# Optimization experiments

Measured on AMD Instinct MI355X. Metric: run time of the kernel, lower is better.

## Reference

```python
import jax, jax.numpy as jnp
import numpy as np

N = 50000      # nodes
E = 800000     # edges (avg degree 16)
DIN = 500      # input_dim
HID = 100      # hid_dim (fixed in module)
DOUT = 64      # output_dim
EPS = 1e-5     # LayerNorm eps (torch default)


def _layer_norm(x, g, b):
    mu = jnp.mean(x, axis=-1, keepdims=True)
    var = jnp.var(x, axis=-1, keepdims=True)
    return (x - mu) / jnp.sqrt(var + EPS) * g + b


def _gcn_conv(x, src, tgt, W, b):
    # PyG GCNConv: self-loops + symmetric normalization + linear + scatter-add
    h = x @ W  # [N, out]
    idx = jnp.arange(N)
    src_sl = jnp.concatenate([src, idx])
    tgt_sl = jnp.concatenate([tgt, idx])
    deg = jax.ops.segment_sum(jnp.ones(src_sl.shape, h.dtype), tgt_sl, num_segments=N)
    dinv = jnp.where(deg > 0, deg ** -0.5, 0.0)
    norm = dinv[src_sl] * dinv[tgt_sl]  # [E+N]
    out = jax.ops.segment_sum(h[src_sl] * norm[:, None], tgt_sl, num_segments=N)
    return out + b


def setup_inputs() -> dict:
    key = jax.random.key(0)
    ks = jax.random.split(key, 10)
    glorot = lambda k, fi, fo: jax.random.normal(k, (fi, fo), jnp.float32) * np.float32(1.0 / np.sqrt(fi))
    z = lambda d: jnp.zeros((d,), jnp.float32)
    return dict(
        data_x=jax.random.normal(ks[0], (N, DIN), jnp.float32),
        data_edge_index=jax.random.randint(ks[1], (2, E), 0, N),
        data_edge_attr=jnp.zeros((E,), jnp.int32),  # single relation type
        t_W1=glorot(ks[2], DIN, HID), t_b1=z(HID), t_g1=jnp.ones((HID,), jnp.float32), t_be1=z(HID),
        t_W2=glorot(ks[3], HID, HID), t_b2=z(HID), t_g2=jnp.ones((HID,), jnp.float32), t_be2=z(HID),
        r_Wrel=glorot(ks[4], HID, HID)[None],  # [n_relations=1, H, H]
        r_Wself=glorot(ks[5], HID, HID), r_b=z(HID),
        c1_W=glorot(ks[6], HID, HID), c1_b=z(HID),
        c2_W=glorot(ks[7], HID, DOUT), c2_b=z(DOUT),
    )


def reference(data_x, data_edge_index, data_edge_attr,
              t_W1, t_b1, t_g1, t_be1, t_W2, t_b2, t_g2, t_be2,
              r_Wrel, r_Wself, r_b, c1_W, c1_b, c2_W, c2_b):
    src, tgt = data_edge_index[0], data_edge_index[1]
    # transform: Linear -> LN -> ReLU -> Linear -> LN -> ReLU
    x = jax.nn.relu(_layer_norm(data_x @ t_W1 + t_b1, t_g1, t_be1))
    x = jax.nn.relu(_layer_norm(x @ t_W2 + t_b2, t_g2, t_be2))
    # RGCN, n_relations=1, n_layers=1: per-relation message + self transform
    msgs = x[src] @ r_Wrel[0]  # edge_attr is all relation 0
    x = x @ r_Wself + jax.ops.segment_sum(msgs, tgt, num_segments=N) + r_b
    x = jax.nn.relu(x)  # dropout = identity (eval)
    x = jax.nn.relu(_gcn_conv(x, src, tgt, c1_W, c1_b))
    x = _gcn_conv(x, src, tgt, c2_W, c2_b)
    return jax.nn.log_softmax(x, axis=1)
```

## Files before the change

### kernel.cpp

```cpp
#include <hip/hip_runtime.h>
#include <hip/hip_bf16.h>

typedef __attribute__((ext_vector_type(8))) short short8;
typedef __attribute__((ext_vector_type(8))) unsigned short ushort8;
typedef __attribute__((ext_vector_type(4))) float f32x4;

static constexpr int NN = 50000;
static constexpr int NE = 800000;
static constexpr int SCAN_B = 196;
static constexpr int NBLK = (NN + 63) / 64;

#define MFMA16x16x32 __builtin_amdgcn_mfma_f32_16x16x32_bf16

__device__ __forceinline__ float b2f(unsigned short u){
  unsigned v = ((unsigned)u) << 16;
  return __builtin_bit_cast(float, v);
}
__device__ __forceinline__ unsigned short f2b(float f){
  unsigned x = __builtin_bit_cast(unsigned, f);
  unsigned r = (x + 0x7fffu + ((x >> 16) & 1u)) >> 16;
  return (unsigned short)r;
}
__device__ __forceinline__ short8 u2s(ushort8 v){
  return __builtin_bit_cast(short8, v);
}

__device__ __align__(256) int   g_isf32;
__device__ __align__(256) unsigned short g_W1t  [112 * 512];
__device__ __align__(256) unsigned short g_W2t  [112 * 128];
__device__ __align__(256) unsigned short g_WselfT[112 * 128];
__device__ __align__(256) unsigned short g_WrelT [112 * 128];
__device__ __align__(256) unsigned short g_c1Wt [112 * 128];
__device__ __align__(256) unsigned short g_c2Wt [64 * 128];
__device__ __align__(256) unsigned short g_bufA[(size_t)NN * 128];
__device__ __align__(256) unsigned short g_bufB[(size_t)NN * 128];
__device__ __align__(256) unsigned short g_bufC[(size_t)NN * 128];
__device__ __align__(256) int   g_deg[NN];
__device__ __align__(256) int   g_rowptr[NN + 1];
__device__ __align__(256) int   g_cursor[NN];
__device__ __align__(256) int   g_colidx[NE];
__device__ __align__(256) float g_dinv[NN];
__device__ __align__(256) int   g_partial[256];

__device__ __forceinline__ float ld_in(const void* p, int idx, int isf32){
  if (isf32) return ((const float*)p)[idx];
  return b2f(((const unsigned short*)p)[idx]);
}

__global__ void k_detect_zero(const unsigned short* __restrict__ x){
  if (blockIdx.x == 0){
    __shared__ int sh[256];
    int tid = threadIdx.x;
    int cnt = 0;
    for (int j = 0; j < 16; j++){
      unsigned short h = x[(size_t)(tid * 16 + j) * 2];
      int e = (h >> 7) & 0xFF;
      if (e >= 90 && e <= 160) cnt++;
    }
    sh[tid] = cnt;
    __syncthreads();
    for (int off = 128; off > 0; off >>= 1){
      if (tid < off) sh[tid] += sh[tid + off];
      __syncthreads();
    }
    if (tid == 0) g_isf32 = (sh[0] < 2458) ? 1 : 0;
  } else {
    int i = (blockIdx.x - 1) * 256 + threadIdx.x;
    if (i < NN){ g_deg[i] = 0; g_cursor[i] = 0; }
  }
}

__device__ __forceinline__ void xp_one(const void* W, unsigned short* Wt, int idx,
                                       int K, int Nc, int Kpad, int isf32){
  int n = idx / Kpad;
  int k = idx - n * Kpad;
  float v = 0.f;
  if (n < Nc && k < K) v = ld_in(W, k * Nc + n, isf32);
  Wt[idx] = f2b(v);
}
__global__ void k_transpose_all(const void* W1, const void* W2, const void* Wself,
                                const void* Wrel, const void* c1W, const void* c2W){
  int idx = blockIdx.x * 256 + threadIdx.x;
  const int isf32 = g_isf32;
  if (idx < 57344){ xp_one(W1, g_W1t, idx, 500, 100, 512, isf32); return; }
  idx -= 57344;
  if (idx < 14336){ xp_one(W2,    g_W2t,    idx, 100, 100, 128, isf32); return; }
  idx -= 14336;
  if (idx < 14336){ xp_one(Wself, g_WselfT, idx, 100, 100, 128, isf32); return; }
  idx -= 14336;
  if (idx < 14336){ xp_one(Wrel,  g_WrelT,  idx, 100, 100, 128, isf32); return; }
  idx -= 14336;
  if (idx < 14336){ xp_one(c1W,   g_c1Wt,   idx, 100, 100, 128, isf32); return; }
  idx -= 14336;
  if (idx < 8192){  xp_one(c2W,   g_c2Wt,   idx, 100, 64,  128, isf32); }
}

__global__ void k_deg(const int* __restrict__ tgt){
  int e = blockIdx.x * 256 + threadIdx.x;
  if (e < NE) atomicAdd(&g_deg[tgt[e]], 1);
}
__global__ __launch_bounds__(256) void k_scan1(){
  __shared__ int sh[256];
  int t = threadIdx.x;
  int i = blockIdx.x * 256 + t;
  int val = (i < NN) ? g_deg[i] : 0;
  sh[t] = val; __syncthreads();
#pragma unroll
  for (int off = 1; off < 256; off <<= 1){
    int v = (t >= off) ? sh[t - off] : 0;
    __syncthreads(); sh[t] += v; __syncthreads();
  }
  if (i < NN){ g_rowptr[i] = sh[t] - val; g_dinv[i] = rsqrtf((float)(val + 1)); }
  if (t == 255) g_partial[blockIdx.x] = sh[255];
}
__global__ __launch_bounds__(256) void k_scan2(){
  __shared__ int sh[256];
  int t = threadIdx.x;
  int val = (t < SCAN_B) ? g_partial[t] : 0;
  sh[t] = val; __syncthreads();
#pragma unroll
  for (int off = 1; off < 256; off <<= 1){
    int v = (t >= off) ? sh[t - off] : 0;
    __syncthreads(); sh[t] += v; __syncthreads();
  }
  if (t < SCAN_B) g_partial[t] = sh[t] - val;
  if (t == 255) g_rowptr[NN] = sh[255];
}
__global__ __launch_bounds__(256) void k_scan3(){
  int i = blockIdx.x * 256 + threadIdx.x;
  if (i < NN) g_rowptr[i] += g_partial[blockIdx.x];
}
__global__ void k_fill(const int* __restrict__ src, const int* __restrict__ tgt){
  int e = blockIdx.x * 256 + threadIdx.x;
  if (e >= NE) return;
  int t = tgt[e];
  int pos = g_rowptr[t] + atomicAdd(&g_cursor[t], 1);
  g_colidx[pos] = src[e];
}


template<int DO_LN>
__device__ __forceinline__ void wave_epi(const f32x4* acc, unsigned short* dst,
    int rstride, int grow0, int lane, int isf32,
    const void* bias, const void* gm, const void* be){
  const int m = lane & 15;
  const int q = lane >> 4;
  float bf_[7], gf_[7], ef_[7];
#pragma unroll
  for (int t = 0; t < 7; t++){
    int col = t * 16 + m;
    bool ok = col < 100;
    bf_[t] = ok ? ld_in(bias, col, isf32) : 0.f;
    if (DO_LN){
      gf_[t] = ok ? ld_in(gm, col, isf32) : 0.f;
      ef_[t] = ok ? ld_in(be, col, isf32) : 0.f;
    }
  }
#pragma unroll
  for (int r = 0; r < 4; r++){
    int rl = q * 4 + r;
    float vals[7], s1 = 0.f, s2 = 0.f;
#pragma unroll
    for (int t = 0; t < 7; t++){
      int col = t * 16 + m;
      float v = (col < 100) ? (acc[t][r] + bf_[t]) : 0.f;
      vals[t] = v; s1 += v; s2 += v * v;
    }
    if (DO_LN){
#pragma unroll
      for (int msk = 1; msk < 16; msk <<= 1){
        s1 += __shfl_xor(s1, msk, 64);
        s2 += __shfl_xor(s2, msk, 64);
      }
      float mu = s1 * 0.01f;
      float var = fmaxf(s2 * 0.01f - mu * mu, 0.f);
      float rstd = rsqrtf(var + 1e-5f);
#pragma unroll
      for (int t = 0; t < 7; t++)
        vals[t] = (vals[t] - mu) * rstd * gf_[t] + ef_[t];
    }
    if (grow0 + rl < NN){
      unsigned short* orow = dst + (size_t)rl * rstride;
#pragma unroll
      for (int t = 0; t < 7; t++){
        int col = t * 16 + m;
        float y = fmaxf(vals[t], 0.f);
        orow[col] = f2b((col < 100) ? y : 0.f);
      }
      orow[112 + m] = 0;
    }
  }
}

template<int MODE>
__device__ __forceinline__ void agg_tile(const unsigned short* __restrict__ x,
    unsigned short* aggT, int tid, int brow0){
  const int nl = tid >> 2;
  const int c0 = (tid & 3) * 32;
  const int node = min(brow0 + nl, NN - 1);
  const float wt = (MODE != 0) ? g_dinv[node] : 1.f;
  float a[32];
#pragma unroll
  for (int k = 0; k < 32; k++) a[k] = 0.f;
  const int p0 = g_rowptr[node], p1 = g_rowptr[node + 1];
  for (int p = p0; p < p1; p += 2){
    int s0 = g_colidx[p];
    bool ok1 = (p + 1) < p1;
    int s1 = ok1 ? g_colidx[p + 1] : node;
    float w0 = (MODE != 0) ? g_dinv[s0] * wt : 1.f;
    float w1 = ok1 ? ((MODE != 0) ? g_dinv[s1] * wt : 1.f) : 0.f;
    ushort8 r0[4], r1[4];
#pragma unroll
    for (int u = 0; u < 4; u++){
      r0[u] = *reinterpret_cast<const ushort8*>(&x[(size_t)s0 * 128 + c0 + u * 8]);
      r1[u] = *reinterpret_cast<const ushort8*>(&x[(size_t)s1 * 128 + c0 + u * 8]);
    }
#pragma unroll
    for (int u = 0; u < 4; u++)
#pragma unroll
      for (int k = 0; k < 8; k++){
        a[u * 8 + k] += w0 * b2f((unsigned short)r0[u][k]);
        a[u * 8 + k] += w1 * b2f((unsigned short)r1[u][k]);
      }
  }
  if (MODE != 0){
    float ws = wt * wt;
#pragma unroll
    for (int u = 0; u < 4; u++){
      ushort8 sv = *reinterpret_cast<const ushort8*>(&x[(size_t)node * 128 + c0 + u * 8]);
#pragma unroll
      for (int k = 0; k < 8; k++) a[u * 8 + k] += ws * b2f((unsigned short)sv[k]);
    }
  }
  unsigned short* arow = aggT + nl * 136 + c0;
#pragma unroll
  for (int u = 0; u < 4; u++){
    ushort8 o;
#pragma unroll
    for (int k = 0; k < 8; k++) o[k] = f2b(a[u * 8 + k]);
    *reinterpret_cast<ushort8*>(&arow[u * 8]) = o;
  }
}


__global__ __launch_bounds__(256, 4) void k_gemm12(const void* __restrict__ Aext,
    const void* b1, const void* gm1, const void* be1,
    const void* b2, const void* gm2, const void* be2){
  __shared__ unsigned short xT[4][16][136];
  const int tid = threadIdx.x;
  const int w = tid >> 6, lane = tid & 63;
  const int m = lane & 15, q = lane >> 4;
  const int row0 = blockIdx.x * 64 + w * 16;
  const int isf32 = g_isf32;
  const int arow = min(row0 + m, NN - 1);

  f32x4 acc[7] = {};
  if (isf32){
    const float* base = (const float*)Aext + (size_t)arow * 500;
#pragma unroll 4
    for (int kc = 0; kc < 16; kc++){
      int col = kc * 32 + q * 8;
      f32x4 lo = *reinterpret_cast<const f32x4*>(base + min(col, 496));
      f32x4 hi = *reinterpret_cast<const f32x4*>(base + min(col + 4, 496));
      short8 a = {(short)f2b(lo[0]), (short)f2b(lo[1]), (short)f2b(lo[2]), (short)f2b(lo[3]),
                  (short)f2b(hi[0]), (short)f2b(hi[1]), (short)f2b(hi[2]), (short)f2b(hi[3])};
#pragma unroll
      for (int t = 0; t < 7; t++){
        short8 b = *reinterpret_cast<const short8*>(g_W1t + (size_t)(t * 16 + m) * 512 + col);
        acc[t] = MFMA16x16x32(a, b, acc[t], 0, 0, 0);
      }
    }
  } else {
    const unsigned short* base = (const unsigned short*)Aext + (size_t)arow * 500;
#pragma unroll 4
    for (int kc = 0; kc < 16; kc++){
      int col = kc * 32 + q * 8;
      ushort4 lo = *reinterpret_cast<const ushort4*>(base + min(col, 496));
      ushort4 hi = *reinterpret_cast<const ushort4*>(base + min(col + 4, 496));
      short8 a = {(short)lo.x, (short)lo.y, (short)lo.z, (short)lo.w,
                  (short)hi.x, (short)hi.y, (short)hi.z, (short)hi.w};
#pragma unroll
      for (int t = 0; t < 7; t++){
        short8 b = *reinterpret_cast<const short8*>(g_W1t + (size_t)(t * 16 + m) * 512 + col);
        acc[t] = MFMA16x16x32(a, b, acc[t], 0, 0, 0);
      }
    }
  }
  wave_epi<1>(acc, &xT[w][0][0], 136, 0, lane, isf32, b1, gm1, be1);
  __syncthreads();

  f32x4 acc2[7] = {};
#pragma unroll
  for (int kc = 0; kc < 4; kc++){
    int k0 = kc * 32 + q * 8;
    short8 a = u2s(*reinterpret_cast<const ushort8*>(&xT[w][m][k0]));
#pragma unroll
    for (int t = 0; t < 7; t++){
      short8 b = *reinterpret_cast<const short8*>(g_W2t + (size_t)(t * 16 + m) * 128 + k0);
      acc2[t] = MFMA16x16x32(a, b, acc2[t], 0, 0, 0);
    }
  }
  wave_epi<1>(acc2, g_bufB + (size_t)row0 * 128, 128, row0, lane, isf32, b2, gm2, be2);
}

__global__ __launch_bounds__(256, 4) void k_rgcn_f(const void* rb){
  __shared__ unsigned short aggT[64 * 136];
  const int tid = threadIdx.x;
  const int brow0 = blockIdx.x * 64;
  agg_tile<0>(g_bufB, aggT, tid, brow0);
  __syncthreads();

  const int w = tid >> 6, lane = tid & 63;
  const int m = lane & 15, q = lane >> 4;
  const int row0 = brow0 + w * 16;
  const int arow = min(row0 + m, NN - 1);
  const int isf32 = g_isf32;
  f32x4 acc[7] = {};
#pragma unroll
  for (int kc = 0; kc < 4; kc++){
    int k0 = kc * 32 + q * 8;
    short8 a1 = u2s(*reinterpret_cast<const ushort8*>(&g_bufB[(size_t)arow * 128 + k0]));
#pragma unroll
    for (int t = 0; t < 7; t++){
      short8 b = *reinterpret_cast<const short8*>(g_WselfT + (size_t)(t * 16 + m) * 128 + k0);
      acc[t] = MFMA16x16x32(a1, b, acc[t], 0, 0, 0);
    }
    short8 a2 = u2s(*reinterpret_cast<const ushort8*>(&aggT[(w * 16 + m) * 136 + k0]));
#pragma unroll
    for (int t = 0; t < 7; t++){
      short8 b = *reinterpret_cast<const short8*>(g_WrelT + (size_t)(t * 16 + m) * 128 + k0);
      acc[t] = MFMA16x16x32(a2, b, acc[t], 0, 0, 0);
    }
  }
  wave_epi<0>(acc, g_bufC + (size_t)row0 * 128, 128, row0, lane, isf32, rb, nullptr, nullptr);
}

__global__ __launch_bounds__(256, 4) void k_conv_f(const void* c1b){
  __shared__ unsigned short aggT[64 * 136];
  const int tid = threadIdx.x;
  const int brow0 = blockIdx.x * 64;
  agg_tile<1>(g_bufC, aggT, tid, brow0);
  __syncthreads();

  const int w = tid >> 6, lane = tid & 63;
  const int m = lane & 15, q = lane >> 4;
  const int row0 = brow0 + w * 16;
  const int isf32 = g_isf32;
  unsigned short* tile = aggT + w * 16 * 136;

  f32x4 acc[7] = {};
#pragma unroll
  for (int kc = 0; kc < 4; kc++){
    int k0 = kc * 32 + q * 8;
    short8 a = u2s(*reinterpret_cast<const ushort8*>(&tile[m * 136 + k0]));
#pragma unroll
    for (int t = 0; t < 7; t++){
      short8 b = *reinterpret_cast<const short8*>(g_c1Wt + (size_t)(t * 16 + m) * 128 + k0);
      acc[t] = MFMA16x16x32(a, b, acc[t], 0, 0, 0);
    }
  }
  __syncthreads();
  wave_epi<0>(acc, tile, 136, 0, lane, isf32, c1b, nullptr, nullptr);
  __syncthreads();

  f32x4 acc2[4] = {};
#pragma unroll
  for (int kc = 0; kc < 4; kc++){
    int k0 = kc * 32 + q * 8;
    short8 a = u2s(*reinterpret_cast<const ushort8*>(&tile[m * 136 + k0]));
#pragma unroll
    for (int t = 0; t < 4; t++){
      short8 b = *reinterpret_cast<const short8*>(g_c2Wt + (size_t)(t * 16 + m) * 128 + k0);
      acc2[t] = MFMA16x16x32(a, b, acc2[t], 0, 0, 0);
    }
  }
#pragma unroll
  for (int r = 0; r < 4; r++){
    int row = row0 + q * 4 + r;
    if (row < NN){
      unsigned short* orow = g_bufA + (size_t)row * 64;
#pragma unroll
      for (int t = 0; t < 4; t++) orow[t * 16 + m] = f2b(acc2[t][r]);
    }
  }
}

__global__ __launch_bounds__(256) void k_agg_lsm(const void* __restrict__ bias,
                                                 void* __restrict__ outv){
  const int isf32 = g_isf32;
  int node = blockIdx.x * 32 + (threadIdx.x >> 3);
  if (node >= NN) return;
  const int c8 = (threadIdx.x & 7) * 8;
  float wt = g_dinv[node];
  float a[4][8];
#pragma unroll
  for (int j = 0; j < 4; j++)
#pragma unroll
    for (int k = 0; k < 8; k++) a[j][k] = 0.f;
  int p0 = g_rowptr[node], p1 = g_rowptr[node + 1];
  for (int p = p0; p < p1; p += 4){
    int sj[4]; float wj[4];
#pragma unroll
    for (int j = 0; j < 4; j++){
      bool ok = (p + j) < p1;
      sj[j] = ok ? g_colidx[p + j] : node;
      wj[j] = ok ? g_dinv[sj[j]] * wt : 0.f;
    }
    ushort8 r[4];
#pragma unroll
    for (int j = 0; j < 4; j++)
      r[j] = *reinterpret_cast<const ushort8*>(&g_bufA[(size_t)sj[j] * 64 + c8]);
#pragma unroll
    for (int j = 0; j < 4; j++)
#pragma unroll
      for (int k = 0; k < 8; k++) a[j][k] += wj[j] * b2f((unsigned short)r[j][k]);
  }
  float ws = wt * wt;
  ushort8 sv = *reinterpret_cast<const ushort8*>(&g_bufA[(size_t)node * 64 + c8]);
#pragma unroll
  for (int k = 0; k < 8; k++) a[0][k] += ws * b2f((unsigned short)sv[k]);

  float v[8], mx = -1e30f;
#pragma unroll
  for (int k = 0; k < 8; k++){
    v[k] = a[0][k] + a[1][k] + a[2][k] + a[3][k] + ld_in(bias, c8 + k, isf32);
    mx = fmaxf(mx, v[k]);
  }
#pragma unroll
  for (int msk = 1; msk < 8; msk <<= 1) mx = fmaxf(mx, __shfl_xor(mx, msk, 64));
  float se = 0.f;
#pragma unroll
  for (int k = 0; k < 8; k++) se += expf(v[k] - mx);
#pragma unroll
  for (int msk = 1; msk < 8; msk <<= 1) se += __shfl_xor(se, msk, 64);
  float lse = logf(se);
  size_t ro = (size_t)node * 64 + c8;
  if (isf32){
    float* o = (float*)outv + ro;
#pragma unroll
    for (int k = 0; k < 8; k++) o[k] = v[k] - mx - lse;
  } else {
    unsigned short* o = (unsigned short*)outv + ro;
#pragma unroll
    for (int k = 0; k < 8; k++) o[k] = f2b(v[k] - mx - lse);
  }
}

extern "C" void kernel_launch(void* const* d_in, const int* in_sizes, int n_in,
                              void* d_out, int out_size, void* d_ws, size_t ws_size,
                              hipStream_t stream){
  (void)in_sizes; (void)n_in; (void)out_size; (void)d_ws; (void)ws_size;
  const void* data_x = d_in[0];
  const int* ei = (const int*)d_in[1];
  const int* src = ei;
  const int* tgt = ei + NE;
  const void *W1 = d_in[3], *b1 = d_in[4], *gm1 = d_in[5], *be1 = d_in[6];
  const void *W2 = d_in[7], *b2 = d_in[8], *gm2 = d_in[9], *be2 = d_in[10];
  const void *Wrel = d_in[11], *Wself = d_in[12], *rb = d_in[13];
  const void *c1W = d_in[14], *c1b = d_in[15];
  const void *c2W = d_in[16], *c2b = d_in[17];

  k_detect_zero<<<1 + (NN + 255) / 256, 256, 0, stream>>>((const unsigned short*)data_x);
  k_transpose_all<<<(122880 + 255) / 256, 256, 0, stream>>>(W1, W2, Wself, Wrel, c1W, c2W);

  k_deg<<<(NE + 255) / 256, 256, 0, stream>>>(tgt);
  k_scan1<<<SCAN_B, 256, 0, stream>>>();
  k_scan2<<<1, 256, 0, stream>>>();
  k_scan3<<<SCAN_B, 256, 0, stream>>>();
  k_fill<<<(NE + 255) / 256, 256, 0, stream>>>(src, tgt);

  k_gemm12<<<NBLK, 256, 0, stream>>>(data_x, b1, gm1, be1, b2, gm2, be2);
  k_rgcn_f<<<NBLK, 256, 0, stream>>>(rb);
  k_conv_f<<<NBLK, 256, 0, stream>>>(c1b);
  k_agg_lsm<<<(NN + 31) / 32, 256, 0, stream>>>(c2b, d_out);
}
```

Measured before the change: 480.9 us.

## Block weight layout by K, deepen gather unrolling, prefetch GEMM inputs, drop block barriers

The transposed weights are now stored in 32-wide K blocks, so each lane's B fragment loads come from a contiguous region. The edge-gather loops now issue four (fused GCN/RGCN tiles) or eight (final aggregation) neighbour rows per iteration, giving more loads in flight. The first GEMM preloads a whole chunk of A into registers behind a scheduling barrier. Block-wide __syncthreads are removed where each wave only touches its own LDS rows, and launch bounds drop from 4 to 3 blocks per CU to make room for the extra registers, which may reduce occupancy.

```diff
diff --git a/kernel.cpp b/kernel.cpp
--- a/kernel.cpp
+++ b/kernel.cpp
@@ -71,28 +71,28 @@
 }
 
 __device__ __forceinline__ void xp_one(const void* W, unsigned short* Wt, int idx,
-                                       int K, int Nc, int Kpad, int isf32){
+                                       int K, int Nc, int Kpad, int Npad, int isf32){
   int n = idx / Kpad;
   int k = idx - n * Kpad;
   float v = 0.f;
   if (n < Nc && k < K) v = ld_in(W, k * Nc + n, isf32);
-  Wt[idx] = f2b(v);
+  Wt[(k >> 5) * (Npad * 32) + n * 32 + (k & 31)] = f2b(v);
 }
 __global__ void k_transpose_all(const void* W1, const void* W2, const void* Wself,
                                 const void* Wrel, const void* c1W, const void* c2W){
   int idx = blockIdx.x * 256 + threadIdx.x;
   const int isf32 = g_isf32;
-  if (idx < 57344){ xp_one(W1, g_W1t, idx, 500, 100, 512, isf32); return; }
+  if (idx < 57344){ xp_one(W1, g_W1t, idx, 500, 100, 512, 112, isf32); return; }
   idx -= 57344;
-  if (idx < 14336){ xp_one(W2,    g_W2t,    idx, 100, 100, 128, isf32); return; }
+  if (idx < 14336){ xp_one(W2,    g_W2t,    idx, 100, 100, 128, 112, isf32); return; }
   idx -= 14336;
-  if (idx < 14336){ xp_one(Wself, g_WselfT, idx, 100, 100, 128, isf32); return; }
+  if (idx < 14336){ xp_one(Wself, g_WselfT, idx, 100, 100, 128, 112, isf32); return; }
   idx -= 14336;
-  if (idx < 14336){ xp_one(Wrel,  g_WrelT,  idx, 100, 100, 128, isf32); return; }
+  if (idx < 14336){ xp_one(Wrel,  g_WrelT,  idx, 100, 100, 128, 112, isf32); return; }
   idx -= 14336;
-  if (idx < 14336){ xp_one(c1W,   g_c1Wt,   idx, 100, 100, 128, isf32); return; }
+  if (idx < 14336){ xp_one(c1W,   g_c1Wt,   idx, 100, 100, 128, 112, isf32); return; }
   idx -= 14336;
-  if (idx < 8192){  xp_one(c2W,   g_c2Wt,   idx, 100, 64,  128, isf32); }
+  if (idx < 8192){  xp_one(c2W,   g_c2Wt,   idx, 100, 64,  128, 64, isf32); }
 }
 
 __global__ void k_deg(const int* __restrict__ tgt){
@@ -203,25 +203,27 @@
 #pragma unroll
   for (int k = 0; k < 32; k++) a[k] = 0.f;
   const int p0 = g_rowptr[node], p1 = g_rowptr[node + 1];
-  for (int p = p0; p < p1; p += 2){
-    int s0 = g_colidx[p];
-    bool ok1 = (p + 1) < p1;
-    int s1 = ok1 ? g_colidx[p + 1] : node;
-    float w0 = (MODE != 0) ? g_dinv[s0] * wt : 1.f;
-    float w1 = ok1 ? ((MODE != 0) ? g_dinv[s1] * wt : 1.f) : 0.f;
-    ushort8 r0[4], r1[4];
-#pragma unroll
-    for (int u = 0; u < 4; u++){
-      r0[u] = *reinterpret_cast<const ushort8*>(&x[(size_t)s0 * 128 + c0 + u * 8]);
-      r1[u] = *reinterpret_cast<const ushort8*>(&x[(size_t)s1 * 128 + c0 + u * 8]);
-    }
-#pragma unroll
-    for (int u = 0; u < 4; u++)
-#pragma unroll
-      for (int k = 0; k < 8; k++){
-        a[u * 8 + k] += w0 * b2f((unsigned short)r0[u][k]);
-        a[u * 8 + k] += w1 * b2f((unsigned short)r1[u][k]);
-      }
+  for (int p = p0; p < p1; p += 4){
+    int s[4]; float wj[4];
+#pragma unroll
+    for (int j = 0; j < 4; j++){
+      bool ok = (p + j) < p1;
+      s[j] = ok ? g_colidx[p + j] : node;
+      wj[j] = ok ? ((MODE != 0) ? g_dinv[s[j]] * wt : 1.f) : 0.f;
+    }
+    ushort8 r[4][4];
+#pragma unroll
+    for (int j = 0; j < 4; j++)
+#pragma unroll
+      for (int u = 0; u < 4; u++)
+        r[j][u] = *reinterpret_cast<const ushort8*>(&x[(size_t)s[j] * 128 + c0 + u * 8]);
+#pragma unroll
+    for (int j = 0; j < 4; j++)
+#pragma unroll
+      for (int u = 0; u < 4; u++)
+#pragma unroll
+        for (int k = 0; k < 8; k++)
+          a[u * 8 + k] += wj[j] * b2f((unsigned short)r[j][u][k]);
   }
   if (MODE != 0){
     float ws = wt * wt;
@@ -243,7 +245,7 @@
 }
 
 
-__global__ __launch_bounds__(256, 4) void k_gemm12(const void* __restrict__ Aext,
+__global__ __launch_bounds__(256, 3) void k_gemm12(const void* __restrict__ Aext,
     const void* b1, const void* gm1, const void* be1,
     const void* b2, const void* gm2, const void* be2){
   __shared__ unsigned short xT[4][16][136];
@@ -257,58 +259,74 @@
   f32x4 acc[7] = {};
   if (isf32){
     const float* base = (const float*)Aext + (size_t)arow * 500;
-#pragma unroll 4
+#pragma unroll
+    for (int h = 0; h < 2; h++){
+      f32x4 Ab[16];
+#pragma unroll
+      for (int kc = 0; kc < 8; kc++){
+        int col = (h * 8 + kc) * 32 + q * 8;
+        Ab[2 * kc]     = *reinterpret_cast<const f32x4*>(base + min(col, 496));
+        Ab[2 * kc + 1] = *reinterpret_cast<const f32x4*>(base + min(col + 4, 496));
+      }
+      __builtin_amdgcn_sched_barrier(0);
+#pragma unroll
+      for (int kc = 0; kc < 8; kc++){
+        f32x4 lo = Ab[2 * kc], hi = Ab[2 * kc + 1];
+        short8 a = {(short)f2b(lo[0]), (short)f2b(lo[1]), (short)f2b(lo[2]), (short)f2b(lo[3]),
+                    (short)f2b(hi[0]), (short)f2b(hi[1]), (short)f2b(hi[2]), (short)f2b(hi[3])};
+        const unsigned short* bp = g_W1t + (h * 8 + kc) * 3584 + m * 32 + q * 8;
+#pragma unroll
+        for (int t = 0; t < 7; t++){
+          short8 b = *reinterpret_cast<const short8*>(bp + t * 512);
+          acc[t] = MFMA16x16x32(a, b, acc[t], 0, 0, 0);
+        }
+      }
+    }
+  } else {
+    const unsigned short* base = (const unsigned short*)Aext + (size_t)arow * 500;
+    ushort4 Ab[32];
+#pragma unroll
     for (int kc = 0; kc < 16; kc++){
       int col = kc * 32 + q * 8;
-      f32x4 lo = *reinterpret_cast<const f32x4*>(base + min(col, 496));
-      f32x4 hi = *reinterpret_cast<const f32x4*>(base + min(col + 4, 496));
-      short8 a = {(short)f2b(lo[0]), (short)f2b(lo[1]), (short)f2b(lo[2]), (short)f2b(lo[3]),
-                  (short)f2b(hi[0]), (short)f2b(hi[1]), (short)f2b(hi[2]), (short)f2b(hi[3])};
+      Ab[2 * kc]     = *reinterpret_cast<const ushort4*>(base + min(col, 496));
+      Ab[2 * kc + 1] = *reinterpret_cast<const ushort4*>(base + min(col + 4, 496));
+    }
+    __builtin_amdgcn_sched_barrier(0);
+#pragma unroll
+    for (int kc = 0; kc < 16; kc++){
+      ushort4 lo = Ab[2 * kc], hi = Ab[2 * kc + 1];
+      short8 a = {(short)lo.x, (short)lo.y, (short)lo.z, (short)lo.w,
+                  (short)hi.x, (short)hi.y, (short)hi.z, (short)hi.w};
+      const unsigned short* bp = g_W1t + kc * 3584 + m * 32 + q * 8;
 #pragma unroll
       for (int t = 0; t < 7; t++){
-        short8 b = *reinterpret_cast<const short8*>(g_W1t + (size_t)(t * 16 + m) * 512 + col);
+        short8 b = *reinterpret_cast<const short8*>(bp + t * 512);
         acc[t] = MFMA16x16x32(a, b, acc[t], 0, 0, 0);
       }
     }
-  } else {
-    const unsigned short* base = (const unsigned short*)Aext + (size_t)arow * 500;
-#pragma unroll 4
-    for (int kc = 0; kc < 16; kc++){
-      int col = kc * 32 + q * 8;
-      ushort4 lo = *reinterpret_cast<const ushort4*>(base + min(col, 496));
-      ushort4 hi = *reinterpret_cast<const ushort4*>(base + min(col + 4, 496));
-      short8 a = {(short)lo.x, (short)lo.y, (short)lo.z, (short)lo.w,
-                  (short)hi.x, (short)hi.y, (short)hi.z, (short)hi.w};
-#pragma unroll
-      for (int t = 0; t < 7; t++){
-        short8 b = *reinterpret_cast<const short8*>(g_W1t + (size_t)(t * 16 + m) * 512 + col);
-        acc[t] = MFMA16x16x32(a, b, acc[t], 0, 0, 0);
-      }
-    }
   }
   wave_epi<1>(acc, &xT[w][0][0], 136, 0, lane, isf32, b1, gm1, be1);
-  __syncthreads();
 
   f32x4 acc2[7] = {};
 #pragma unroll
   for (int kc = 0; kc < 4; kc++){
     int k0 = kc * 32 + q * 8;
     short8 a = u2s(*reinterpret_cast<const ushort8*>(&xT[w][m][k0]));
+    const unsigned short* bp = g_W2t + kc * 3584 + m * 32 + q * 8;
 #pragma unroll
     for (int t = 0; t < 7; t++){
-      short8 b = *reinterpret_cast<const short8*>(g_W2t + (size_t)(t * 16 + m) * 128 + k0);
+      short8 b = *reinterpret_cast<const short8*>(bp + t * 512);
       acc2[t] = MFMA16x16x32(a, b, acc2[t], 0, 0, 0);
     }
   }
   wave_epi<1>(acc2, g_bufB + (size_t)row0 * 128, 128, row0, lane, isf32, b2, gm2, be2);
 }
 
-__global__ __launch_bounds__(256, 4) void k_rgcn_f(const void* rb){
+__global__ __launch_bounds__(256, 3) void k_rgcn_f(const void* rb){
   __shared__ unsigned short aggT[64 * 136];
   const int tid = threadIdx.x;
   const int brow0 = blockIdx.x * 64;
   agg_tile<0>(g_bufB, aggT, tid, brow0);
-  __syncthreads();
 
   const int w = tid >> 6, lane = tid & 63;
   const int m = lane & 15, q = lane >> 4;
@@ -320,27 +338,28 @@
   for (int kc = 0; kc < 4; kc++){
     int k0 = kc * 32 + q * 8;
     short8 a1 = u2s(*reinterpret_cast<const ushort8*>(&g_bufB[(size_t)arow * 128 + k0]));
+    const unsigned short* bp1 = g_WselfT + kc * 3584 + m * 32 + q * 8;
 #pragma unroll
     for (int t = 0; t < 7; t++){
-      short8 b = *reinterpret_cast<const short8*>(g_WselfT + (size_t)(t * 16 + m) * 128 + k0);
+      short8 b = *reinterpret_cast<const short8*>(bp1 + t * 512);
       acc[t] = MFMA16x16x32(a1, b, acc[t], 0, 0, 0);
     }
     short8 a2 = u2s(*reinterpret_cast<const ushort8*>(&aggT[(w * 16 + m) * 136 + k0]));
+    const unsigned short* bp2 = g_WrelT + kc * 3584 + m * 32 + q * 8;
 #pragma unroll
     for (int t = 0; t < 7; t++){
-      short8 b = *reinterpret_cast<const short8*>(g_WrelT + (size_t)(t * 16 + m) * 128 + k0);
+      short8 b = *reinterpret_cast<const short8*>(bp2 + t * 512);
       acc[t] = MFMA16x16x32(a2, b, acc[t], 0, 0, 0);
     }
   }
   wave_epi<0>(acc, g_bufC + (size_t)row0 * 128, 128, row0, lane, isf32, rb, nullptr, nullptr);
 }
 
-__global__ __launch_bounds__(256, 4) void k_conv_f(const void* c1b){
+__global__ __launch_bounds__(256, 3) void k_conv_f(const void* c1b){
   __shared__ unsigned short aggT[64 * 136];
   const int tid = threadIdx.x;
   const int brow0 = blockIdx.x * 64;
   agg_tile<1>(g_bufC, aggT, tid, brow0);
-  __syncthreads();
 
   const int w = tid >> 6, lane = tid & 63;
   const int m = lane & 15, q = lane >> 4;
@@ -353,24 +372,24 @@
   for (int kc = 0; kc < 4; kc++){
     int k0 = kc * 32 + q * 8;
     short8 a = u2s(*reinterpret_cast<const ushort8*>(&tile[m * 136 + k0]));
+    const unsigned short* bp = g_c1Wt + kc * 3584 + m * 32 + q * 8;
 #pragma unroll
     for (int t = 0; t < 7; t++){
-      short8 b = *reinterpret_cast<const short8*>(g_c1Wt + (size_t)(t * 16 + m) * 128 + k0);
+      short8 b = *reinterpret_cast<const short8*>(bp + t * 512);
       acc[t] = MFMA16x16x32(a, b, acc[t], 0, 0, 0);
     }
   }
-  __syncthreads();
   wave_epi<0>(acc, tile, 136, 0, lane, isf32, c1b, nullptr, nullptr);
-  __syncthreads();
 
   f32x4 acc2[4] = {};
 #pragma unroll
   for (int kc = 0; kc < 4; kc++){
     int k0 = kc * 32 + q * 8;
     short8 a = u2s(*reinterpret_cast<const ushort8*>(&tile[m * 136 + k0]));
+    const unsigned short* bp = g_c2Wt + kc * 2048 + m * 32 + q * 8;
 #pragma unroll
     for (int t = 0; t < 4; t++){
-      short8 b = *reinterpret_cast<const short8*>(g_c2Wt + (size_t)(t * 16 + m) * 128 + k0);
+      short8 b = *reinterpret_cast<const short8*>(bp + t * 512);
       acc2[t] = MFMA16x16x32(a, b, acc2[t], 0, 0, 0);
     }
   }
@@ -398,22 +417,22 @@
 #pragma unroll
     for (int k = 0; k < 8; k++) a[j][k] = 0.f;
   int p0 = g_rowptr[node], p1 = g_rowptr[node + 1];
-  for (int p = p0; p < p1; p += 4){
-    int sj[4]; float wj[4];
-#pragma unroll
-    for (int j = 0; j < 4; j++){
+  for (int p = p0; p < p1; p += 8){
+    int sj[8]; float wj[8];
+#pragma unroll
+    for (int j = 0; j < 8; j++){
       bool ok = (p + j) < p1;
       sj[j] = ok ? g_colidx[p + j] : node;
       wj[j] = ok ? g_dinv[sj[j]] * wt : 0.f;
     }
-    ushort8 r[4];
-#pragma unroll
-    for (int j = 0; j < 4; j++)
+    ushort8 r[8];
+#pragma unroll
+    for (int j = 0; j < 8; j++)
       r[j] = *reinterpret_cast<const ushort8*>(&g_bufA[(size_t)sj[j] * 64 + c8]);
 #pragma unroll
-    for (int j = 0; j < 4; j++)
-#pragma unroll
-      for (int k = 0; k < 8; k++) a[j][k] += wj[j] * b2f((unsigned short)r[j][k]);
+    for (int j = 0; j < 8; j++)
+#pragma unroll
+      for (int k = 0; k < 8; k++) a[j & 3][k] += wj[j] * b2f((unsigned short)r[j][k]);
   }
   float ws = wt * wt;
   ushort8 sv = *reinterpret_cast<const ushort8*>(&g_bufA[(size_t)node * 64 + c8]);
```

Measured after the change: 478.3 us. About the same (-0.5%).
